# Kernel optimization log

Measured on AMD Instinct MI355X. Metric: run time of the kernel, lower is better.

Reference implementation:

```python
import math
import jax, jax.numpy as jnp
import numpy as np
from jax import lax

# FPN anchor layout: 1024x768 image, strides {4,8,16,32,64}, 3 anchors/location
NUM_PER_LEVEL = (147456, 36864, 9216, 2304, 576)
A_TOTAL = sum(NUM_PER_LEVEL)
BATCH = 8
PRE_NMS_TOP_N = 1000   # testing
POST_NMS_TOP_N = 1000  # testing
NMS_THRESH = 0.7
SCORE_THRESH = 0.0
MIN_SIZE = 1.0
IMG_H, IMG_W = 768.0, 1024.0
BBOX_XFORM_CLIP = math.log(1000.0 / 16.0)


def setup_inputs() -> dict:
    key = jax.random.key(0)
    k1, k2, k3, k4, k5, k6 = jax.random.split(key, 6)
    objectness = jax.random.normal(k1, (BATCH, A_TOTAL), jnp.float32)
    pred_bbox_deltas = jax.random.normal(k2, (BATCH, A_TOTAL, 4), jnp.float32) * 0.2
    # valid anchor boxes (x1, y1, x2, y2)
    cx = jax.random.uniform(k3, (A_TOTAL,), jnp.float32) * IMG_W
    cy = jax.random.uniform(k4, (A_TOTAL,), jnp.float32) * IMG_H
    w = 16.0 + jax.random.uniform(k5, (A_TOTAL,), jnp.float32) * 176.0
    h = 16.0 + jax.random.uniform(k6, (A_TOTAL,), jnp.float32) * 176.0
    anchors = jnp.stack([cx - 0.5 * w, cy - 0.5 * h, cx + 0.5 * w, cy + 0.5 * h], -1)
    return {"objectness": objectness, "pred_bbox_deltas": pred_bbox_deltas, "anchors": anchors}


def _nms_image(boxes, scores, lvl, valid):
    """batched_nms (level-offset trick) + post-NMS top-k, fixed shapes.
    boxes [K,4], scores [K], lvl [K] int, valid [K] bool -> [POST_NMS_TOP_N, 5]"""
    K = boxes.shape[0]
    s = jnp.where(valid, scores, -1.0)
    order = jnp.argsort(-s)  # decreasing score (invalid last)
    b = boxes[order]
    s = s[order]
    v = valid[order]
    # offset boxes per level so cross-level boxes never overlap (torchvision batched_nms)
    offset = lvl[order].astype(b.dtype) * (jnp.max(lax.stop_gradient(boxes)) + 1.0)
    nb = lax.stop_gradient(b) + offset[:, None]
    area = (nb[:, 2] - nb[:, 0]) * (nb[:, 3] - nb[:, 1])
    lt = jnp.maximum(nb[:, None, :2], nb[None, :, :2])  # [K,K,2]
    rb = jnp.minimum(nb[:, None, 2:], nb[None, :, 2:])
    wh = jnp.clip(rb - lt, 0.0)
    inter = wh[..., 0] * wh[..., 1]
    iou = inter / jnp.maximum(area[:, None] + area[None, :] - inter, 1e-9)
    pos = jnp.arange(K)

    def body(keep, i):
        sup = keep[i] & (iou[i] > NMS_THRESH) & (pos > i)
        return keep & ~sup, None

    keep, _ = lax.scan(body, v, pos)
    masked = jnp.where(keep, s, -1.0)
    top_s, top_i = lax.top_k(masked, POST_NMS_TOP_N)  # kept, decreasing score
    sel_b = b[top_i]
    ok = top_s > -0.5
    sel_b = jnp.where(ok[:, None], sel_b, 0.0)
    top_s = jnp.where(ok, top_s, 0.0)
    return jnp.concatenate([sel_b, top_s[:, None]], axis=-1)


def reference(objectness, pred_bbox_deltas, anchors):
    # --- box decode (BoxCoder, weights (1,1,1,1)) ---
    wa = anchors[:, 2] - anchors[:, 0]
    ha = anchors[:, 3] - anchors[:, 1]
    cxa = anchors[:, 0] + 0.5 * wa
    cya = anchors[:, 1] + 0.5 * ha
    dx, dy = pred_bbox_deltas[..., 0], pred_bbox_deltas[..., 1]
    dw = jnp.minimum(pred_bbox_deltas[..., 2], BBOX_XFORM_CLIP)
    dh = jnp.minimum(pred_bbox_deltas[..., 3], BBOX_XFORM_CLIP)
    pcx = dx * wa + cxa
    pcy = dy * ha + cya
    pw = jnp.exp(dw) * wa
    ph = jnp.exp(dh) * ha
    proposals = jnp.stack(
        [pcx - 0.5 * pw, pcy - 0.5 * ph, pcx + 0.5 * pw, pcy + 0.5 * ph], axis=-1
    )  # [B, A, 4]

    # --- per-level pre-NMS top-k (_get_top_n_idx) ---
    levels = jnp.concatenate(
        [jnp.full((n,), i, jnp.int32) for i, n in enumerate(NUM_PER_LEVEL)]
    )
    idx_parts = []
    off = 0
    for n in NUM_PER_LEVEL:
        k = min(PRE_NMS_TOP_N, n)
        _, ti = lax.top_k(objectness[:, off:off + n], k)
        idx_parts.append(ti + off)
        off += n
    top_idx = jnp.concatenate(idx_parts, axis=1)  # [B, K]

    scores = jax.nn.sigmoid(jnp.take_along_axis(objectness, top_idx, axis=1))
    lvl = levels[top_idx]
    boxes = jnp.take_along_axis(proposals, top_idx[..., None], axis=1)  # [B,K,4]

    # --- clip to image ---
    x1 = jnp.clip(boxes[..., 0], 0.0, IMG_W)
    y1 = jnp.clip(boxes[..., 1], 0.0, IMG_H)
    x2 = jnp.clip(boxes[..., 2], 0.0, IMG_W)
    y2 = jnp.clip(boxes[..., 3], 0.0, IMG_H)
    boxes = jnp.stack([x1, y1, x2, y2], axis=-1)

    # remove_small_boxes + score threshold (as validity mask; fixed shapes)
    valid = ((x2 - x1) >= MIN_SIZE) & ((y2 - y1) >= MIN_SIZE) & (scores >= SCORE_THRESH)

    # --- per-image batched NMS + post-NMS top-k ---
    return jax.vmap(_nms_image)(boxes, scores, lvl, valid)  # [B, POST_NMS_TOP_N, 5]
```

## Files before the change

### kernel.cpp

```cpp
#include <hip/hip_runtime.h>
#include <math.h>

#pragma clang fp contract(off)

#define A_TOTAL 196416
#define BATCH 8
#define KTOT 4576
#define NLEV 5
#define MSPLIT 16
#define RCAP 6144
#define NPARTS 12

static __device__ const int d_aoff[NLEV] = {0, 147456, 184320, 193536, 195840};
static __device__ const int d_n[NLEV]    = {147456, 36864, 9216, 2304, 576};
static __device__ const int d_k[NLEV]    = {1000, 1000, 1000, 1000, 576};
static __device__ const int d_spl[NLEV]  = {8, 2, 1, 1, 1};
static __device__ const int d_bp[NLEV]   = {0, 8, 10, 11, 12};
static __device__ const int d_pb_l[13]    = {0,0,0,0,0,0,0,0,1,1,2,3,4};
static __device__ const int d_pb_part[13] = {0,1,2,3,4,5,6,7,0,1,0,0,0};

#define TM_IOU (0.699999988079071044921875 + 0x1p-25)

__device__ inline unsigned int mono(float f) {
  unsigned int u = __float_as_uint(f);
  return (u & 0x80000000u) ? ~u : (u | 0x80000000u);
}
__device__ inline float imono(unsigned int m) {
  return __uint_as_float((m & 0x80000000u) ? (m & 0x7FFFFFFFu) : ~m);
}

__device__ inline int cnt_gt(const float* A, int n, float s) {
  int lo = 0, hi = n;
  while (lo < hi) { int mid = (lo + hi) >> 1; if (A[mid] > s) lo = mid + 1; else hi = mid; }
  return lo;
}
__device__ inline int cnt_ge(const float* A, int n, float s) {
  int lo = 0, hi = n;
  while (lo < hi) { int mid = (lo + hi) >> 1; if (A[mid] >= s) lo = mid + 1; else hi = mid; }
  return lo;
}

__global__ __launch_bounds__(1024) void k_hist(const float* __restrict__ obj,
                                               int* __restrict__ hist_g,
                                               int* __restrict__ cnt_g,
                                               float* __restrict__ maxblk,
                                               unsigned long long* __restrict__ keepbits,
                                               int* __restrict__ done) {
  int blk = blockIdx.x;
  int tid = threadIdx.x;
  if (blk == 0) {
    for (int i = tid; i < 40 * NPARTS; i += 1024) maxblk[i] = 0.0f;
    for (int i = tid; i < 40; i += 1024) cnt_g[i] = 0;
    for (int i = tid; i < 40 * 16; i += 1024) keepbits[i] = 0ull;
    if (tid < BATCH) done[tid] = 0;
  }
  int b = blk / 13, pb = blk % 13;
  int l = d_pb_l[pb], part = d_pb_part[pb];
  int slice = d_n[l] / d_spl[l];
  int start = d_aoff[l] + part * slice;
  const float4* p4 = (const float4*)(obj + (size_t)b * A_TOTAL + start);
  int s4 = slice >> 2;
  __shared__ int h[4096];
  for (int i = tid; i < 4096; i += 1024) h[i] = 0;
  __syncthreads();
  for (int i = tid; i < s4; i += 1024) {
    float4 v = p4[i];
    atomicAdd(&h[mono(v.x) >> 20], 1);
    atomicAdd(&h[mono(v.y) >> 20], 1);
    atomicAdd(&h[mono(v.z) >> 20], 1);
    atomicAdd(&h[mono(v.w) >> 20], 1);
  }
  __syncthreads();
  int* outp = hist_g + (size_t)blk * 4096;
  for (int i = tid; i < 4096; i += 1024) outp[i] = h[i];
}

__global__ __launch_bounds__(1024) void k_collect(const float* __restrict__ obj,
                                                  const int* __restrict__ hist_g,
                                                  int* __restrict__ cnt_g,
                                                  unsigned long long* __restrict__ cand_g) {
  int blk = blockIdx.x;
  int b = blk / 13, pb = blk % 13;
  int l = d_pb_l[pb], part = d_pb_part[pb];
  int bl = b * NLEV + l;
  const int k = d_k[l];
  int tid = threadIdx.x, lane = tid & 63;
  __shared__ int t[4096];
  __shared__ int grp[256];
  __shared__ unsigned int sP;
  __shared__ __align__(16) unsigned long long lbuf[RCAP];
  __shared__ int s_cnt, s_base;
  int parts = d_spl[l];
  const int* hb = hist_g + (size_t)(b * 13 + d_bp[l]) * 4096;
  for (int bin = tid; bin < 4096; bin += 1024) {
    int s = 0;
    for (int p = 0; p < parts; ++p) s += hb[p * 4096 + bin];
    t[bin] = s;
  }
  if (tid == 0) s_cnt = 0;
  __syncthreads();
  if (tid < 256) {
    int s = 0;
    for (int j = 0; j < 16; ++j) s += t[tid * 16 + j];
    grp[tid] = s;
  }
  __syncthreads();
  if (tid == 0) {
    int cum = 0, g, d;
    for (g = 255; g >= 0; --g) {
      if (cum + grp[g] >= k) break;
      cum += grp[g];
    }
    for (d = 15; d >= 0; --d) {
      int c = t[g * 16 + d];
      if (cum + c >= k) break;
      cum += c;
    }
    sP = (unsigned int)(g * 16 + d);
  }
  __syncthreads();
  unsigned int P = sP;
  int slice = d_n[l] / parts;
  int start = d_aoff[l] + part * slice;
  const float4* p4 = (const float4*)(obj + (size_t)b * A_TOTAL + start);
  int s4 = slice >> 2;
  int lbase = part * slice;
  for (int i = tid; i < s4; i += 1024) {
    float4 v = p4[i];
    unsigned int a[4] = {mono(v.x), mono(v.y), mono(v.z), mono(v.w)};
    bool q0 = (a[0] >> 20) >= P, q1 = (a[1] >> 20) >= P;
    bool q2 = (a[2] >> 20) >= P, q3 = (a[3] >> 20) >= P;
    if (__ballot(q0 | q1 | q2 | q3)) {
      bool qs[4] = {q0, q1, q2, q3};
#pragma unroll
      for (int c = 0; c < 4; ++c) {
        unsigned long long mb = __ballot(qs[c]);
        if (mb) {
          int base;
          if (lane == 0) base = atomicAdd(&s_cnt, __popcll(mb));
          base = __shfl(base, 0);
          if (qs[c]) {
            int slot = base + __popcll(mb & ((1ull << lane) - 1ull));
            if (slot < RCAP) {
              int idx = lbase + 4 * i + c;
              lbuf[slot] = ((unsigned long long)a[c] << 32) |
                           (unsigned int)(~(unsigned int)idx);
            }
          }
        }
      }
    }
  }
  __syncthreads();
  int cnt = min(s_cnt, RCAP);
  if (tid == 0) s_base = atomicAdd(&cnt_g[bl], cnt);
  __syncthreads();
  int base = s_base;
  for (int i = tid; i < cnt; i += 1024) {
    int slot = base + i;
    if (slot < RCAP) cand_g[(size_t)bl * RCAP + slot] = lbuf[i];
  }
}

__device__ inline float decode_emit(unsigned long long e, int rank, int b,
                                    int k, int aoff, int bl,
                                    const float* __restrict__ deltas,
                                    const float* __restrict__ anchors,
                                    float* __restrict__ sc0,
                                    float4* __restrict__ box0) {
  if (rank >= k) return 0.0f;
  unsigned int k32 = (unsigned int)(e >> 32);
  unsigned int idx = ~(unsigned int)(e & 0xFFFFFFFFull);
  float o = imono(k32);
  int gidx = aoff + (int)idx;
  const float* dl = deltas + ((size_t)b * A_TOTAL + gidx) * 4;
  const float* an = anchors + (size_t)gidx * 4;
  float a0 = an[0], a1 = an[1], a2 = an[2], a3 = an[3];
  float wa = a2 - a0, ha = a3 - a1;
  float cxa = a0 + 0.5f * wa, cya = a1 + 0.5f * ha;
  float dx = dl[0], dy = dl[1];
  const float CLIPV = 4.135166556742356f;
  float dw = fminf(dl[2], CLIPV), dh = fminf(dl[3], CLIPV);
  float pcx = dx * wa + cxa;
  float pcy = dy * ha + cya;
  float pw = (float)exp((double)dw) * wa;
  float ph = (float)exp((double)dh) * ha;
  float x1 = pcx - 0.5f * pw, y1 = pcy - 0.5f * ph;
  float x2 = pcx + 0.5f * pw, y2 = pcy + 0.5f * ph;
  x1 = fminf(fmaxf(x1, 0.0f), 1024.0f);
  x2 = fminf(fmaxf(x2, 0.0f), 1024.0f);
  y1 = fminf(fmaxf(y1, 0.0f), 768.0f);
  y2 = fminf(fmaxf(y2, 0.0f), 768.0f);
  float s = (float)(1.0 / (1.0 + exp(-(double)o)));
  bool valid = ((x2 - x1) >= 1.0f) && ((y2 - y1) >= 1.0f) && (s >= 0.0f);
  sc0[bl * 1024 + rank] = valid ? s : -1.0f;
  box0[bl * 1024 + rank] = make_float4(x1, y1, x2, y2);
  return fmaxf(fmaxf(x1, y1), fmaxf(x2, y2));
}

__global__ __launch_bounds__(256) void k_rankdec(const unsigned long long* __restrict__ cand_g,
                                                 const int* __restrict__ cnt_g,
                                                 const float* __restrict__ deltas,
                                                 const float* __restrict__ anchors,
                                                 float* __restrict__ sc0,
                                                 float4* __restrict__ box0,
                                                 float* __restrict__ maxblk) {
  int bl = blockIdx.x / NPARTS, part = blockIdx.x % NPARTS;
  int b = bl / NLEV, l = bl % NLEV;
  const int k = d_k[l], aoff = d_aoff[l];
  int cnt = min(cnt_g[bl], RCAP);
  if (part * 512 >= cnt) return;
  __shared__ __align__(16) unsigned long long cb[RCAP];
  __shared__ unsigned int s_max;
  int tid = threadIdx.x;
  if (tid == 0) s_max = 0u;
  const unsigned long long* src = cand_g + (size_t)bl * RCAP;
  {
    const ulonglong2* s2 = (const ulonglong2*)src;
    ulonglong2* d2 = (ulonglong2*)cb;
    int n2 = cnt >> 1;
    for (int i = tid; i < n2; i += 256) d2[i] = s2[i];
    if ((cnt & 1) && tid == 0) cb[cnt - 1] = src[cnt - 1];
  }
  __syncthreads();
  int i0 = part * 512 + tid, i1 = i0 + 256;
  unsigned long long e0 = ~0ull, e1 = ~0ull;
  if (i0 < cnt) e0 = cb[i0];
  if (i1 < cnt) e1 = cb[i1];
  int r0 = 0, r1 = 0;
  int nc2 = cnt >> 1;
  const ulonglong2* c2 = (const ulonglong2*)cb;
  for (int j = 0; j < nc2; ++j) {
    ulonglong2 v = c2[j];
    r0 += (v.x > e0) + (v.y > e0);
    r1 += (v.x > e1) + (v.y > e1);
  }
  if (cnt & 1) {
    unsigned long long v = cb[cnt - 1];
    r0 += (v > e0);
    r1 += (v > e1);
  }
  float mx = 0.0f;
  if (i0 < cnt) mx = fmaxf(mx, decode_emit(e0, r0, b, k, aoff, bl, deltas, anchors, sc0, box0));
  if (i1 < cnt) mx = fmaxf(mx, decode_emit(e1, r1, b, k, aoff, bl, deltas, anchors, sc0, box0));
#pragma unroll
  for (int s = 1; s < 64; s <<= 1) mx = fmaxf(mx, __shfl_xor(mx, s));
  if ((tid & 63) == 0) atomicMax(&s_max, __float_as_uint(mx));
  __syncthreads();
  if (tid == 0) maxblk[blockIdx.x] = __uint_as_float(s_max);
}

__global__ __launch_bounds__(1024) void k_mask(const float* __restrict__ sc0,
                                               const float4* __restrict__ box0,
                                               const float* __restrict__ maxblk,
                                               float* __restrict__ lvlsc,
                                               float4* __restrict__ lvlraw,
                                               int* __restrict__ g_V,
                                               unsigned long long* __restrict__ masks) {
  int blk = blockIdx.x;
  int bl = blk / MSPLIT, part = blk % MSPLIT;
  int b = bl / NLEV, l = bl % NLEV;
  const int k = d_k[l];
  int tid = threadIdx.x, lane = tid & 63, w = tid >> 6;
  __shared__ float4 lbox[1024];
  __shared__ float s_mv;
  __shared__ int s_wcnt[16];
  if (w == 0) {
    float v = 0.0f;
    for (int i = lane; i < NLEV * NPARTS; i += 64)
      v = fmaxf(v, maxblk[b * (NLEV * NPARTS) + i]);
#pragma unroll
    for (int s = 1; s < 64; s <<= 1) v = fmaxf(v, __shfl_xor(v, s));
    if (lane == 0) s_mv = v;
  }
  bool in = tid < k;
  float s = in ? sc0[bl * 1024 + tid] : -1.0f;
  bool valid = in && (s >= 0.0f);
  unsigned long long mb = __ballot(valid);
  if (lane == 0) s_wcnt[w] = __popcll(mb);
  __syncthreads();
  int pre = 0;
  for (int ww = 0; ww < w; ++ww) pre += s_wcnt[ww];
  int j = pre + __popcll(mb & ((1ull << lane) - 1ull));
  int V = 0;
  for (int ww = 0; ww < 16; ++ww) V += s_wcnt[ww];
  float off = (float)l * (s_mv + 1.0f);
  if (valid) {
    float4 bx = box0[bl * 1024 + tid];
    lbox[j] = make_float4(bx.x + off, bx.y + off, bx.z + off, bx.w + off);
    if (part == 0) {
      lvlsc[bl * 1024 + j] = s;
      lvlraw[bl * 1024 + j] = bx;
    }
  }
  if (part == 0 && tid == 0) g_V[bl] = V;
  __syncthreads();
  int row0 = part * 64;
  if (row0 >= V) return;
  int i = row0 + lane;
  if (i >= V) return;
  float4 bb = lbox[i];
  float ba = (bb.z - bb.x) * (bb.w - bb.y);
  unsigned long long bits = 0ull;
  int jbase = w * 64;
  if (jbase + 63 > i && jbase < V) {
    int jhi = min(64, V - jbase);
    for (int jo = 0; jo < jhi; ++jo) {
      int jj = jbase + jo;
      float4 cb = lbox[jj];
      float ca = (cb.z - cb.x) * (cb.w - cb.y);
      float xx1 = fmaxf(bb.x, cb.x), yy1 = fmaxf(bb.y, cb.y);
      float xx2 = fminf(bb.z, cb.z), yy2 = fminf(bb.w, cb.w);
      float wd = fmaxf(xx2 - xx1, 0.0f), ht = fmaxf(yy2 - yy1, 0.0f);
      float inter = wd * ht;
      float denom = fmaxf(ba + ca - inter, 1e-9f);
      if ((jj > i) && ((double)inter >= TM_IOU * (double)denom)) bits |= (1ull << jo);
    }
  }
  masks[((size_t)bl * 16 + w) * 1024 + i] = bits;
}

__global__ __launch_bounds__(1024) void k_scanout(const unsigned long long* __restrict__ masks,
                                                  const int* __restrict__ g_V,
                                                  unsigned long long* __restrict__ keepbits,
                                                  const float* __restrict__ lvlsc,
                                                  const float4* __restrict__ lvlraw,
                                                  int* __restrict__ done,
                                                  float* __restrict__ out) {
  int bl = blockIdx.x;
  int b = bl / NLEV, l = bl % NLEV;
  int tid = threadIdx.x, lane = tid & 63, w = tid >> 6;
  int V = g_V[bl];
  const int nch = (V + 63) / 64;
  const unsigned long long* M = masks + (size_t)bl * 16 * 1024;
  __shared__ unsigned long long s_remv[16];
  __shared__ unsigned long long s_D[2][72];
  __shared__ unsigned long long s_dw;
  if (tid < 16) s_remv[tid] = ~0ull;
  int base_w = w * 64;
  unsigned long long init_w;
  if (V <= base_w) init_w = ~0ull;
  else if (V >= base_w + 64) init_w = 0ull;
  else init_w = (~0ull) << (V - base_w);
  if (w == 0 && nch > 0) s_D[0][lane] = (lane < V) ? M[lane] : 0ull;
  if (tid < 8) { s_D[0][64 + tid] = 0ull; s_D[1][64 + tid] = 0ull; }
  unsigned long long acc = 0ull;
  __syncthreads();

  for (int c = 0; c < nch; ++c) {
    unsigned long long val = 0ull;
    int r = 64 * c + lane;
    if (w > c && w < nch && r < V) val = M[(size_t)w * 1024 + r];
    if (w == c) {
      unsigned long long red = acc;
#pragma unroll
      for (int s = 1; s < 64; s <<= 1) red |= __shfl_xor(red, s);
      unsigned long long dw = init_w | red;
      const unsigned long long* D = s_D[c & 1];
      unsigned long long pb[8];
#pragma unroll
      for (int u = 0; u < 8; ++u) pb[u] = D[u];
#pragma unroll
      for (int g = 0; g < 8; ++g) {
#pragma unroll
        for (int u = 0; u < 8; ++u) {
          int jj = g * 8 + u;
          if (!((dw >> jj) & 1ull)) dw |= pb[u];
          pb[u] = D[jj + 8];
        }
      }
      if (lane == 0) { s_dw = dw; s_remv[c] = dw; }
    }
    if (w == c + 1 && w < nch) {
      int rr = 64 * (c + 1) + lane;
      s_D[(c + 1) & 1][lane] = (rr < V) ? M[(size_t)(c + 1) * 1024 + rr] : 0ull;
    }
    __syncthreads();
    if (w > c && w < nch) {
      unsigned long long kept = ~s_dw;
      if ((kept >> lane) & 1ull) acc |= val;
    }
    __syncthreads();
  }
  if (tid < 16) {
    unsigned long long kb = ~s_remv[tid];
    if (kb) atomicOr(&keepbits[bl * 16 + tid], kb);
  }
  __threadfence();
  __syncthreads();
  if (tid == 0) atomicAdd(&done[b], 1);
  if (l != 0) return;

  float* ob = out + (size_t)b * 5000;
  for (int i = tid; i < 5000; i += 1024) ob[i] = 0.0f;
  if (tid == 0) {
    while (atomicAdd(&done[b], 0) < NLEV) __builtin_amdgcn_s_sleep(8);
  }
  __syncthreads();

  __shared__ float ksc[NLEV * 1024];
  __shared__ int kj[NLEV * 1024];
  __shared__ int sK[NLEV];
  __shared__ int s_wcnt[16];
  for (int l2 = 0; l2 < NLEV; ++l2) {
    int bl2 = b * NLEV + l2;
    int V2 = g_V[bl2];
    unsigned long long kbw = 0ull;
    if (lane == 0) kbw = atomicAdd(&keepbits[bl2 * 16 + w], 0ull);
    kbw = __shfl(kbw, 0);
    bool kept = (tid < V2) && ((kbw >> lane) & 1ull);
    unsigned long long mb = __ballot(kept);
    if (lane == 0) s_wcnt[w] = __popcll(mb);
    __syncthreads();
    int pre = 0;
    for (int ww = 0; ww < w; ++ww) pre += s_wcnt[ww];
    int r = pre + __popcll(mb & ((1ull << lane) - 1ull));
    if (kept) { ksc[l2 * 1024 + r] = lvlsc[bl2 * 1024 + tid]; kj[l2 * 1024 + r] = tid; }
    if (tid == 0) {
      int t = 0;
      for (int ww = 0; ww < 16; ++ww) t += s_wcnt[ww];
      sK[l2] = t;
    }
    __syncthreads();
  }
  int K[NLEV];
  for (int l2 = 0; l2 < NLEV; ++l2) K[l2] = sK[l2];
  for (int l2 = 0; l2 < NLEV; ++l2) {
    if (tid < K[l2]) {
      float s = ksc[l2 * 1024 + tid];
      int rank = tid;
      for (int l3 = 0; l3 < NLEV; ++l3) {
        if (l3 == l2) continue;
        const float* A = ksc + l3 * 1024;
        rank += (l3 < l2) ? cnt_ge(A, K[l3], s) : cnt_gt(A, K[l3], s);
      }
      if (rank < 1000) {
        float4 bx = lvlraw[(size_t)(b * NLEV + l2) * 1024 + kj[l2 * 1024 + tid]];
        float* op = ob + (size_t)rank * 5;
        op[0] = bx.x; op[1] = bx.y; op[2] = bx.z; op[3] = bx.w; op[4] = s;
      }
    }
  }
}

extern "C" void kernel_launch(void* const* d_in, const int* in_sizes, int n_in,
                              void* d_out, int out_size, void* d_ws, size_t ws_size,
                              hipStream_t stream) {
  const float* obj     = (const float*)d_in[0];
  const float* deltas  = (const float*)d_in[1];
  const float* anchors = (const float*)d_in[2];
  float* out = (float*)d_out;

  char* p = (char*)d_ws;
  float4* box0   = (float4*)p; p += (size_t)40 * 1024 * sizeof(float4);
  float4* lvlraw = (float4*)p; p += (size_t)40 * 1024 * sizeof(float4);
  unsigned long long* cand_g   = (unsigned long long*)p; p += (size_t)40 * RCAP * 8;
  unsigned long long* masks    = (unsigned long long*)p; p += (size_t)40 * 16 * 1024 * 8;
  unsigned long long* keepbits = (unsigned long long*)p; p += (size_t)40 * 16 * 8;
  int*   hist_g = (int*)p;   p += (size_t)104 * 4096 * 4;
  int*   cnt_g  = (int*)p;   p += 40 * 4;
  float* maxblk = (float*)p; p += (size_t)40 * NPARTS * 4;
  float* sc0    = (float*)p; p += (size_t)40 * 1024 * 4;
  float* lvlsc  = (float*)p; p += (size_t)40 * 1024 * 4;
  int*   g_V    = (int*)p;   p += 40 * 4;
  int*   done   = (int*)p;   p += BATCH * 4;

  hipLaunchKernelGGL(k_hist, dim3(BATCH * 13), dim3(1024), 0, stream,
                     obj, hist_g, cnt_g, maxblk, keepbits, done);
  hipLaunchKernelGGL(k_collect, dim3(BATCH * 13), dim3(1024), 0, stream,
                     obj, hist_g, cnt_g, cand_g);
  hipLaunchKernelGGL(k_rankdec, dim3(BATCH * NLEV * NPARTS), dim3(256), 0, stream,
                     cand_g, cnt_g, deltas, anchors, sc0, box0, maxblk);
  hipLaunchKernelGGL(k_mask, dim3(BATCH * NLEV * MSPLIT), dim3(1024), 0, stream,
                     sc0, box0, maxblk, lvlsc, lvlraw, g_V, masks);
  hipLaunchKernelGGL(k_scanout, dim3(BATCH * NLEV), dim3(1024), 0, stream,
                     masks, g_V, keepbits, lvlsc, lvlraw, done, out);
}
```

Before: 213.9 us.

## Split scan/output into separate kernels and prefetch mask rows one chunk ahead

Removes the inter-block spin-wait and atomics in the fused scan+output kernel by splitting it into a per-level scan kernel that compacts kept scores and indices to global memory, followed by a merge kernel. In the merge kernel every level block computes its own ranks, instead of only the level-0 block doing the merge for all five levels. Output zeroing moves into the histogram kernel, and the scan loop software-prefetches the next chunk's mask value. This costs an extra kernel launch and some global round-trips, but spreads the merge across five times as many blocks and removes serialization on the done counter.

```diff
diff --git a/kernel.cpp b/kernel.cpp
--- a/kernel.cpp
+++ b/kernel.cpp
@@ -44,17 +44,18 @@
                                                int* __restrict__ hist_g,
                                                int* __restrict__ cnt_g,
                                                float* __restrict__ maxblk,
-                                               unsigned long long* __restrict__ keepbits,
-                                               int* __restrict__ done) {
+                                               float* __restrict__ out) {
   int blk = blockIdx.x;
   int tid = threadIdx.x;
   if (blk == 0) {
     for (int i = tid; i < 40 * NPARTS; i += 1024) maxblk[i] = 0.0f;
     for (int i = tid; i < 40; i += 1024) cnt_g[i] = 0;
-    for (int i = tid; i < 40 * 16; i += 1024) keepbits[i] = 0ull;
-    if (tid < BATCH) done[tid] = 0;
   }
   int b = blk / 13, pb = blk % 13;
+  if (pb == 0) {
+    float* ob = out + (size_t)b * 5000;
+    for (int i = tid; i < 5000; i += 1024) ob[i] = 0.0f;
+  }
   int l = d_pb_l[pb], part = d_pb_part[pb];
   int slice = d_n[l] / d_spl[l];
   int start = d_aoff[l] + part * slice;
@@ -320,15 +321,13 @@
   masks[((size_t)bl * 16 + w) * 1024 + i] = bits;
 }
 
-__global__ __launch_bounds__(1024) void k_scanout(const unsigned long long* __restrict__ masks,
-                                                  const int* __restrict__ g_V,
-                                                  unsigned long long* __restrict__ keepbits,
-                                                  const float* __restrict__ lvlsc,
-                                                  const float4* __restrict__ lvlraw,
-                                                  int* __restrict__ done,
-                                                  float* __restrict__ out) {
+__global__ __launch_bounds__(1024) void k_scan(const unsigned long long* __restrict__ masks,
+                                               const int* __restrict__ g_V,
+                                               const float* __restrict__ lvlsc,
+                                               float* __restrict__ ksc_g,
+                                               int* __restrict__ kj_g,
+                                               int* __restrict__ K_g) {
   int bl = blockIdx.x;
-  int b = bl / NLEV, l = bl % NLEV;
   int tid = threadIdx.x, lane = tid & 63, w = tid >> 6;
   int V = g_V[bl];
   const int nch = (V + 63) / 64;
@@ -336,6 +335,7 @@
   __shared__ unsigned long long s_remv[16];
   __shared__ unsigned long long s_D[2][72];
   __shared__ unsigned long long s_dw;
+  __shared__ int s_wcnt[16];
   if (tid < 16) s_remv[tid] = ~0ull;
   int base_w = w * 64;
   unsigned long long init_w;
@@ -345,12 +345,15 @@
   if (w == 0 && nch > 0) s_D[0][lane] = (lane < V) ? M[lane] : 0ull;
   if (tid < 8) { s_D[0][64 + tid] = 0ull; s_D[1][64 + tid] = 0ull; }
   unsigned long long acc = 0ull;
+  unsigned long long val_next = 0ull;
+  if (w > 0 && w < nch && lane < V) val_next = M[(size_t)w * 1024 + lane];
   __syncthreads();
 
   for (int c = 0; c < nch; ++c) {
-    unsigned long long val = 0ull;
-    int r = 64 * c + lane;
-    if (w > c && w < nch && r < V) val = M[(size_t)w * 1024 + r];
+    unsigned long long val = val_next;
+    val_next = 0ull;
+    int rn = 64 * (c + 1) + lane;
+    if (w > c + 1 && w < nch && rn < V) val_next = M[(size_t)w * 1024 + rn];
     if (w == c) {
       unsigned long long red = acc;
 #pragma unroll
@@ -382,63 +385,58 @@
     }
     __syncthreads();
   }
-  if (tid < 16) {
-    unsigned long long kb = ~s_remv[tid];
-    if (kb) atomicOr(&keepbits[bl * 16 + tid], kb);
-  }
-  __threadfence();
-  __syncthreads();
-  if (tid == 0) atomicAdd(&done[b], 1);
-  if (l != 0) return;
-
-  float* ob = out + (size_t)b * 5000;
-  for (int i = tid; i < 5000; i += 1024) ob[i] = 0.0f;
+
+  unsigned long long kb = ~s_remv[w];
+  bool kept = ((kb >> lane) & 1ull) != 0ull;
+  unsigned long long mb = __ballot(kept);
+  if (lane == 0) s_wcnt[w] = __popcll(mb);
+  __syncthreads();
+  int pre = 0;
+  for (int ww = 0; ww < w; ++ww) pre += s_wcnt[ww];
+  int r = pre + __popcll(mb & ((1ull << lane) - 1ull));
+  if (kept) {
+    ksc_g[bl * 1024 + r] = lvlsc[bl * 1024 + tid];
+    kj_g[bl * 1024 + r] = tid;
+  }
   if (tid == 0) {
-    while (atomicAdd(&done[b], 0) < NLEV) __builtin_amdgcn_s_sleep(8);
-  }
-  __syncthreads();
-
+    int t = 0;
+    for (int ww = 0; ww < 16; ++ww) t += s_wcnt[ww];
+    K_g[bl] = t;
+  }
+}
+
+__global__ __launch_bounds__(1024) void k_merge(const float* __restrict__ ksc_g,
+                                                const int* __restrict__ kj_g,
+                                                const int* __restrict__ K_g,
+                                                const float4* __restrict__ lvlraw,
+                                                float* __restrict__ out) {
+  int blk = blockIdx.x;
+  int b = blk / NLEV, l = blk % NLEV;
+  int tid = threadIdx.x;
   __shared__ float ksc[NLEV * 1024];
-  __shared__ int kj[NLEV * 1024];
   __shared__ int sK[NLEV];
-  __shared__ int s_wcnt[16];
-  for (int l2 = 0; l2 < NLEV; ++l2) {
-    int bl2 = b * NLEV + l2;
-    int V2 = g_V[bl2];
-    unsigned long long kbw = 0ull;
-    if (lane == 0) kbw = atomicAdd(&keepbits[bl2 * 16 + w], 0ull);
-    kbw = __shfl(kbw, 0);
-    bool kept = (tid < V2) && ((kbw >> lane) & 1ull);
-    unsigned long long mb = __ballot(kept);
-    if (lane == 0) s_wcnt[w] = __popcll(mb);
-    __syncthreads();
-    int pre = 0;
-    for (int ww = 0; ww < w; ++ww) pre += s_wcnt[ww];
-    int r = pre + __popcll(mb & ((1ull << lane) - 1ull));
-    if (kept) { ksc[l2 * 1024 + r] = lvlsc[bl2 * 1024 + tid]; kj[l2 * 1024 + r] = tid; }
-    if (tid == 0) {
-      int t = 0;
-      for (int ww = 0; ww < 16; ++ww) t += s_wcnt[ww];
-      sK[l2] = t;
-    }
-    __syncthreads();
-  }
+  if (tid < NLEV) sK[tid] = K_g[b * NLEV + tid];
+  __syncthreads();
   int K[NLEV];
   for (int l2 = 0; l2 < NLEV; ++l2) K[l2] = sK[l2];
   for (int l2 = 0; l2 < NLEV; ++l2) {
-    if (tid < K[l2]) {
-      float s = ksc[l2 * 1024 + tid];
-      int rank = tid;
-      for (int l3 = 0; l3 < NLEV; ++l3) {
-        if (l3 == l2) continue;
-        const float* A = ksc + l3 * 1024;
-        rank += (l3 < l2) ? cnt_ge(A, K[l3], s) : cnt_gt(A, K[l3], s);
-      }
-      if (rank < 1000) {
-        float4 bx = lvlraw[(size_t)(b * NLEV + l2) * 1024 + kj[l2 * 1024 + tid]];
-        float* op = ob + (size_t)rank * 5;
-        op[0] = bx.x; op[1] = bx.y; op[2] = bx.z; op[3] = bx.w; op[4] = s;
-      }
+    for (int i = tid; i < K[l2]; i += 1024)
+      ksc[l2 * 1024 + i] = ksc_g[(size_t)(b * NLEV + l2) * 1024 + i];
+  }
+  __syncthreads();
+  if (tid < K[l]) {
+    float s = ksc[l * 1024 + tid];
+    int rank = tid;
+    for (int l2 = 0; l2 < NLEV; ++l2) {
+      if (l2 == l) continue;
+      const float* A = ksc + l2 * 1024;
+      rank += (l2 < l) ? cnt_ge(A, K[l2], s) : cnt_gt(A, K[l2], s);
+    }
+    if (rank < 1000) {
+      int j = kj_g[(size_t)(b * NLEV + l) * 1024 + tid];
+      float4 bx = lvlraw[(size_t)(b * NLEV + l) * 1024 + j];
+      float* op = out + (size_t)b * 5000 + (size_t)rank * 5;
+      op[0] = bx.x; op[1] = bx.y; op[2] = bx.z; op[3] = bx.w; op[4] = s;
     }
   }
 }
@@ -454,25 +452,28 @@
   char* p = (char*)d_ws;
   float4* box0   = (float4*)p; p += (size_t)40 * 1024 * sizeof(float4);
   float4* lvlraw = (float4*)p; p += (size_t)40 * 1024 * sizeof(float4);
-  unsigned long long* cand_g   = (unsigned long long*)p; p += (size_t)40 * RCAP * 8;
-  unsigned long long* masks    = (unsigned long long*)p; p += (size_t)40 * 16 * 1024 * 8;
-  unsigned long long* keepbits = (unsigned long long*)p; p += (size_t)40 * 16 * 8;
+  unsigned long long* cand_g = (unsigned long long*)p; p += (size_t)40 * RCAP * 8;
+  unsigned long long* masks  = (unsigned long long*)p; p += (size_t)40 * 16 * 1024 * 8;
   int*   hist_g = (int*)p;   p += (size_t)104 * 4096 * 4;
   int*   cnt_g  = (int*)p;   p += 40 * 4;
   float* maxblk = (float*)p; p += (size_t)40 * NPARTS * 4;
   float* sc0    = (float*)p; p += (size_t)40 * 1024 * 4;
   float* lvlsc  = (float*)p; p += (size_t)40 * 1024 * 4;
   int*   g_V    = (int*)p;   p += 40 * 4;
-  int*   done   = (int*)p;   p += BATCH * 4;
+  float* ksc_g  = (float*)p; p += (size_t)40 * 1024 * 4;
+  int*   kj_g   = (int*)p;   p += (size_t)40 * 1024 * 4;
+  int*   K_g    = (int*)p;   p += 40 * 4;
 
   hipLaunchKernelGGL(k_hist, dim3(BATCH * 13), dim3(1024), 0, stream,
-                     obj, hist_g, cnt_g, maxblk, keepbits, done);
+                     obj, hist_g, cnt_g, maxblk, out);
   hipLaunchKernelGGL(k_collect, dim3(BATCH * 13), dim3(1024), 0, stream,
                      obj, hist_g, cnt_g, cand_g);
   hipLaunchKernelGGL(k_rankdec, dim3(BATCH * NLEV * NPARTS), dim3(256), 0, stream,
                      cand_g, cnt_g, deltas, anchors, sc0, box0, maxblk);
   hipLaunchKernelGGL(k_mask, dim3(BATCH * NLEV * MSPLIT), dim3(1024), 0, stream,
                      sc0, box0, maxblk, lvlsc, lvlraw, g_V, masks);
-  hipLaunchKernelGGL(k_scanout, dim3(BATCH * NLEV), dim3(1024), 0, stream,
-                     masks, g_V, keepbits, lvlsc, lvlraw, done, out);
-}
+  hipLaunchKernelGGL(k_scan, dim3(BATCH * NLEV), dim3(1024), 0, stream,
+                     masks, g_V, lvlsc, ksc_g, kj_g, K_g);
+  hipLaunchKernelGGL(k_merge, dim3(BATCH * NLEV), dim3(1024), 0, stream,
+                     ksc_g, kj_g, K_g, lvlraw, out);
+}
```

New measurement: 197.3 us. 7.8% less time.
